# Performance work log

Measured on AMD Instinct MI355X. Metric: run time of the kernel, lower is better.

Reference implementation:

```python
import jax, jax.numpy as jnp
import numpy as np

HEADS = 8
DIM_HEAD = 64
SCALE = DIM_HEAD ** -0.5


def setup_inputs() -> dict:
    key = jax.random.key(0)
    k1, k2, k3 = jax.random.split(key, 3)
    B, C, L = 4, 512, 2048
    h_dim = HEADS * DIM_HEAD  # 512
    x = jax.random.normal(k1, (B, C, L), dtype=jnp.float32)
    w_qkv = jax.random.normal(k2, (C, 3 * h_dim), dtype=jnp.float32) * (C ** -0.5)
    w_out = jax.random.normal(k3, (h_dim, C), dtype=jnp.float32) * (h_dim ** -0.5)
    b_out = jnp.zeros((C,), dtype=jnp.float32)
    return {"x": x, "w_qkv": w_qkv, "w_out": w_out, "b_out": b_out}


def reference(x, w_qkv, w_out, b_out):
    B, C, L = x.shape
    # pointwise conv (kernel size 1, no bias): [B,C,L] x [C,3hd] -> [B,3hd,L]
    qkv = jnp.einsum('bcl,cf->bfl', x, w_qkv)
    q, k, v = jnp.split(qkv, 3, axis=1)  # each [B, h*d, L]
    def to_heads(t):
        return t.reshape(B, HEADS, DIM_HEAD, L)  # b h d l
    q, k, v = to_heads(q), to_heads(k), to_heads(v)
    q = q * SCALE
    sim = jnp.einsum('bhdi,bhdj->bhij', q, k)  # [B,H,L,L]
    attn = jax.nn.softmax(sim, axis=-1)  # stable (max-subtract) softmax
    out = jnp.einsum('bhij,bhdj->bhid', attn, v)  # [B,H,L,D]
    # rearrange 'b h l c -> b (h c) l'
    out = out.transpose(0, 1, 3, 2).reshape(B, HEADS * DIM_HEAD, L)
    # to_out pointwise conv with bias: [B,hd,L] -> [B,C,L]
    return jnp.einsum('bcl,cf->bfl', out, w_out) + b_out[None, :, None]
```

## Files before the change

kernel.cpp:

```cpp
#include <hip/hip_runtime.h>


#define LDIM 2048
#define CDIM 512
#define BATCH 4

typedef __attribute__((ext_vector_type(8))) short s16x8;
typedef __attribute__((ext_vector_type(4))) float f32x4;
typedef __attribute__((ext_vector_type(4))) unsigned short u16x4;
typedef unsigned int u32;
typedef unsigned short u16;

__device__ __forceinline__ u16 f2b(float f) {
    unsigned u = __float_as_uint(f);
    u += 0x7fffu + ((u >> 16) & 1u);
    return (u16)(u >> 16);
}
__device__ __forceinline__ u32 pk2(float a, float b) {
    u32 ua = __float_as_uint(a) + 0x8000u;
    u32 ub = __float_as_uint(b) + 0x8000u;
    return __builtin_amdgcn_perm(ub, ua, 0x07060302u);
}

__global__ __launch_bounds__(256)
void transpA_k(const float* __restrict__ x, const float* __restrict__ wq,
               const float* __restrict__ wo, u16* __restrict__ XP,
               u16* __restrict__ WP, u16* __restrict__ WOP)
{
    const int r0 = blockIdx.x * 64;
    const int y  = blockIdx.y;
    const float* in; u16* out; int inLD, c0;
    if (y < 128) {
        const int b = y >> 5, ct = y & 31;
        in = x + (size_t)b * CDIM * LDIM; inLD = LDIM; c0 = ct * 64;
        out = XP + (size_t)b * LDIM * CDIM;
    } else if (y < 152) {
        in = wq; inLD = 1536; c0 = (y - 128) * 64; out = WP;
    } else {
        in = wo; inLD = 512;  c0 = (y - 152) * 64; out = WOP;
    }

    __shared__ __align__(16) u16 t[64][80];
    const int tt = threadIdx.x;
    const int lr = tt >> 4, lc = (tt & 15) * 4;
    #pragma unroll
    for (int i = 0; i < 4; ++i) {
        f32x4 v = *(const f32x4*)(in + (size_t)(r0 + lr + i * 16) * inLD + c0 + lc);
        #pragma unroll
        for (int j = 0; j < 4; ++j) t[lc + j][lr + i * 16] = f2b(v[j]);
    }
    __syncthreads();
    const int orow = tt >> 2, ocg = (tt & 3) * 16;
    s16x8 v0 = *(const s16x8*)&t[orow][ocg];
    s16x8 v1 = *(const s16x8*)&t[orow][ocg + 8];
    const int row   = c0 + orow;
    const int rtile = row >> 4, rr = row & 15;
    const int cstep = (r0 + ocg) >> 5;
    const int qb    = (ocg >> 3) & 3;
    u16* dst = out + ((size_t)(rtile * 16 + cstep) * 64 + qb * 16 + rr) * 8;
    *(s16x8*)dst = v0;
    *(s16x8*)(dst + 128) = v1;
}

__global__ __launch_bounds__(256)
void qkvgemm_bf16(const u16* __restrict__ XP, const u16* __restrict__ WP,
                  u16* __restrict__ QF, u16* __restrict__ KF, u16* __restrict__ VF)
{
    const int f0 = blockIdx.x * 64;
    const int l0 = blockIdx.y * 128;
    const int b  = blockIdx.z;
    const u16* xTb = XP + (size_t)b * LDIM * CDIM;
    const int t = threadIdx.x, w = t >> 6, lane = t & 63;
    const int mn = lane & 15, q = lane >> 4;
    const bool vpart = (f0 >= 1024);

    const u16 *Abase, *Bbase;
    int mbase, nbase;
    if (!vpart) {
        mbase = f0 + (w >> 1) * 32; nbase = l0 + (w & 1) * 64;
        Abase = WP + (size_t)mbase * CDIM; Bbase = xTb + (size_t)nbase * CDIM;
    } else {
        mbase = l0 + w * 32; nbase = f0;
        Abase = xTb + (size_t)mbase * CDIM; Bbase = WP + (size_t)nbase * CDIM;
    }

    f32x4 acc[2][4] = {};
    #pragma unroll 2
    for (int c0 = 0; c0 < CDIM; c0 += 32) {
        s16x8 a[2], bf[4];
        #pragma unroll
        for (int mi = 0; mi < 2; ++mi)
            a[mi] = *(const s16x8*)(Abase + mi * 16 * CDIM + c0 * 16 + lane * 8);
        #pragma unroll
        for (int ni = 0; ni < 4; ++ni)
            bf[ni] = *(const s16x8*)(Bbase + ni * 16 * CDIM + c0 * 16 + lane * 8);
        #pragma unroll
        for (int mi = 0; mi < 2; ++mi)
            #pragma unroll
            for (int ni = 0; ni < 4; ++ni)
                acc[mi][ni] = __builtin_amdgcn_mfma_f32_16x16x32_bf16(a[mi], bf[ni], acc[mi][ni], 0, 0, 0);
    }

    if (!vpart) {
        const int part = f0 >> 9;
        const float sc2 = (part == 0) ? 0.18033688f : 1.0f;
        u16* Tout = (part == 0) ? QF : KF;
        #pragma unroll
        for (int mi = 0; mi < 2; ++mi) {
            const int fg0 = mbase + mi * 16;
            const int h = (fg0 >> 6) & 7;
            const int d0 = (fg0 & 63) + q * 4;
            const int kd = d0 >> 5, qq = (d0 >> 3) & 3, e0 = d0 & 7;
            u16* T = Tout + (size_t)(b * 8 + h) * LDIM * 64;
            #pragma unroll
            for (int ni = 0; ni < 4; ++ni) {
                const int lg = nbase + ni * 16 + mn;
                size_t addr;
                if (part == 0) {
                    const int t16 = lg >> 4, mnq = lg & 15;
                    addr = (size_t)((t16 * 2 + kd) * 512 + (qq * 16 + mnq) * 8 + e0);
                } else {
                    const int j64 = lg >> 6, r6 = lg & 63;
                    const int jt  = ((r6 >> 2) & 1) * 2 + (r6 >> 5);
                    const int mnk = ((r6 >> 3) & 3) * 4 + (r6 & 3);
                    addr = (size_t)(((j64 * 4 + jt) * 2 + kd) * 512 + (qq * 16 + mnk) * 8 + e0);
                }
                u16x4 pk;
                #pragma unroll
                for (int r = 0; r < 4; ++r) pk[r] = f2b(acc[mi][ni][r] * sc2);
                *(u16x4*)(T + addr) = pk;
            }
        }
    } else {
        #pragma unroll
        for (int ni = 0; ni < 4; ++ni) {
            const int fg = nbase + ni * 16 + mn;
            const int h = (fg >> 6) & 7;
            const int d = fg & 63;
            const int dt = d >> 4, mnv = d & 15;
            u16* Vb = VF + (size_t)(b * 8 + h) * LDIM * 64;
            #pragma unroll
            for (int mi = 0; mi < 2; ++mi) {
                const int lg0 = mbase + mi * 16 + q * 4;
                const int j64 = lg0 >> 6, j6 = lg0 & 63;
                const int kj = j6 >> 5, qq = (j6 >> 3) & 3, e0 = j6 & 7;
                const size_t addr = (size_t)(((j64 * 2 + kj) * 4 + dt) * 512 + (qq * 16 + mnv) * 8 + e0);
                u16x4 pk;
                #pragma unroll
                for (int r = 0; r < 4; ++r) pk[r] = f2b(acc[mi][ni][r]);
                *(u16x4*)(Vb + addr) = pk;
            }
        }
    }
}

__global__ __launch_bounds__(256)
void attn_k(const u16* __restrict__ QF, const u16* __restrict__ KF,
            const u16* __restrict__ VF, u16* __restrict__ aoP)
{
    const int bh = blockIdx.x;
    const int b = bh >> 3, h = bh & 7;
    const u16* Qh = QF + (size_t)bh * LDIM * 64;
    const u16* Kh = KF + (size_t)bh * LDIM * 64;
    const u16* Vh = VF + (size_t)bh * LDIM * 64;

    __shared__ __align__(16) float o_sh[3][64][68];
    __shared__ float lp_sh[3][64];

    const int tid = threadIdx.x;
    const int wv = tid >> 6;
    const int lane = tid & 63;
    const int mn = lane & 15, q = lane >> 4;
    const int ib64 = blockIdx.y;
    const int TH = 8;
    const int tbase = wv * TH;

    s16x8 aq[4][2];
    #pragma unroll
    for (int ibt = 0; ibt < 4; ++ibt) {
        const int t16 = ib64 * 4 + ibt;
        #pragma unroll
        for (int kd = 0; kd < 2; ++kd)
            aq[ibt][kd] = *(const s16x8*)(Qh + (size_t)((t16 * 2 + kd) * 512) + lane * 8);
    }

    f32x4 o_acc[4][4] = {};
    float lp[4] = {0.f, 0.f, 0.f, 0.f};

    s16x8 kc[2][4];
    {
        const u16* Kt = Kh + (size_t)tbase * 4096;
        #pragma unroll
        for (int kd = 0; kd < 2; ++kd)
            #pragma unroll
            for (int jt = 0; jt < 4; ++jt)
                kc[kd][jt] = *(const s16x8*)(Kt + ((jt * 2 + kd) << 9) + (lane << 3));
    }

    #pragma unroll 2
    for (int jj = 0; jj < TH; ++jj) {
        const int tn = tbase + ((jj + 1) & (TH - 1));
        const u16* Kt = Kh + (size_t)tn * 4096;
        const u16* Vt = Vh + (size_t)(tbase + jj) * 4096;

        s16x8 kn[2][4];
        #pragma unroll
        for (int kd = 0; kd < 2; ++kd)
            #pragma unroll
            for (int jt = 0; jt < 4; ++jt)
                kn[kd][jt] = *(const s16x8*)(Kt + ((jt * 2 + kd) << 9) + (lane << 3));

        f32x4 s[4][4] = {};
        #pragma unroll
        for (int kd = 0; kd < 2; ++kd)
            #pragma unroll
            for (int jt = 0; jt < 4; ++jt)
                #pragma unroll
                for (int ibt = 0; ibt < 4; ++ibt)
                    s[ibt][jt] = __builtin_amdgcn_mfma_f32_16x16x32_bf16(kc[kd][jt], aq[ibt][kd], s[ibt][jt], 0, 0, 0);

        s16x8 vc[2][4];
        #pragma unroll
        for (int kj = 0; kj < 2; ++kj)
            #pragma unroll
            for (int dt = 0; dt < 4; ++dt)
                vc[kj][dt] = *(const s16x8*)(Vt + ((kj * 4 + dt) << 9) + (lane << 3));

        #pragma unroll
        for (int kj = 0; kj < 2; ++kj) {
            s16x8 ap[4];
            #pragma unroll
            for (int ibt = 0; ibt < 4; ++ibt) {
                float pa0 = __builtin_amdgcn_exp2f(s[ibt][kj][0]);
                float pa1 = __builtin_amdgcn_exp2f(s[ibt][kj][1]);
                float pa2 = __builtin_amdgcn_exp2f(s[ibt][kj][2]);
                float pa3 = __builtin_amdgcn_exp2f(s[ibt][kj][3]);
                float pb0 = __builtin_amdgcn_exp2f(s[ibt][kj + 2][0]);
                float pb1 = __builtin_amdgcn_exp2f(s[ibt][kj + 2][1]);
                float pb2 = __builtin_amdgcn_exp2f(s[ibt][kj + 2][2]);
                float pb3 = __builtin_amdgcn_exp2f(s[ibt][kj + 2][3]);
                lp[ibt] += ((pa0 + pa1) + (pa2 + pa3)) + ((pb0 + pb1) + (pb2 + pb3));
                union { s16x8 v; u32 w[4]; } u;
                u.w[0] = pk2(pa0, pa1);
                u.w[1] = pk2(pa2, pa3);
                u.w[2] = pk2(pb0, pb1);
                u.w[3] = pk2(pb2, pb3);
                ap[ibt] = u.v;
            }
            #pragma unroll
            for (int dt = 0; dt < 4; ++dt)
                #pragma unroll
                for (int ibt = 0; ibt < 4; ++ibt)
                    o_acc[ibt][dt] = __builtin_amdgcn_mfma_f32_16x16x32_bf16(vc[kj][dt], ap[ibt], o_acc[ibt][dt], 0, 0, 0);
        }

        #pragma unroll
        for (int kd = 0; kd < 2; ++kd)
            #pragma unroll
            for (int jt = 0; jt < 4; ++jt)
                kc[kd][jt] = kn[kd][jt];
    }

    #pragma unroll
    for (int ibt = 0; ibt < 4; ++ibt) {
        lp[ibt] += __shfl_xor(lp[ibt], 16);
        lp[ibt] += __shfl_xor(lp[ibt], 32);
    }

    if (wv != 0) {
        #pragma unroll
        for (int ibt = 0; ibt < 4; ++ibt) {
            #pragma unroll
            for (int dt = 0; dt < 4; ++dt)
                *(f32x4*)&o_sh[wv - 1][ibt * 16 + mn][dt * 16 + q * 4] = o_acc[ibt][dt];
            if (q == 0) lp_sh[wv - 1][ibt * 16 + mn] = lp[ibt];
        }
    }
    __syncthreads();
    if (wv == 0) {
        u16* Ab = aoP + (size_t)b * LDIM * 512;
        #pragma unroll
        for (int ibt = 0; ibt < 4; ++ibt) {
            const int row = ibt * 16 + mn;
            const float lptot = lp[ibt] + lp_sh[0][row] + lp_sh[1][row] + lp_sh[2][row];
            const float rinv = 1.0f / lptot;
            const int ltile = ib64 * 4 + ibt;
            #pragma unroll
            for (int dt = 0; dt < 4; ++dt) {
                f32x4 o0 = *(const f32x4*)&o_sh[0][row][dt * 16 + q * 4];
                f32x4 o1 = *(const f32x4*)&o_sh[1][row][dt * 16 + q * 4];
                f32x4 o2 = *(const f32x4*)&o_sh[2][row][dt * 16 + q * 4];
                u16x4 pk;
                #pragma unroll
                for (int r = 0; r < 4; ++r)
                    pk[r] = f2b((o_acc[ibt][dt][r] + o0[r] + o1[r] + o2[r]) * rinv);
                const int cstep = h * 2 + (dt >> 1);
                const int lanep = ((dt & 1) * 2 + (q >> 1)) * 16 + mn;
                u16* dst = Ab + ((size_t)(ltile * 16 + cstep) * 64 + lanep) * 8 + (q & 1) * 4;
                *(u16x4*)dst = pk;
            }
        }
    }
}

__global__ __launch_bounds__(256)
void outgemm_d(const u16* __restrict__ aoP, const u16* __restrict__ WOP,
               const float* __restrict__ bias, float* __restrict__ Y)
{
    const int f0 = blockIdx.x * 64;
    const int l0 = blockIdx.y * 128;
    const int b  = blockIdx.z;
    const int t = threadIdx.x, w = t >> 6, lane = t & 63;
    const int mn = lane & 15, q = lane >> 4;
    const int mbase = f0 + (w >> 1) * 32;
    const int nbase = l0 + (w & 1) * 64;
    const u16* Abase = WOP + (size_t)mbase * CDIM;
    const u16* Bbase = aoP + ((size_t)b * LDIM + nbase) * CDIM;
    float* Yb = Y + (size_t)b * CDIM * LDIM;

    f32x4 acc[2][4] = {};
    #pragma unroll 2
    for (int c0 = 0; c0 < CDIM; c0 += 32) {
        s16x8 a[2], bf[4];
        #pragma unroll
        for (int mi = 0; mi < 2; ++mi)
            a[mi] = *(const s16x8*)(Abase + mi * 16 * CDIM + c0 * 16 + lane * 8);
        #pragma unroll
        for (int ni = 0; ni < 4; ++ni)
            bf[ni] = *(const s16x8*)(Bbase + ni * 16 * CDIM + c0 * 16 + lane * 8);
        #pragma unroll
        for (int mi = 0; mi < 2; ++mi)
            #pragma unroll
            for (int ni = 0; ni < 4; ++ni)
                acc[mi][ni] = __builtin_amdgcn_mfma_f32_16x16x32_bf16(a[mi], bf[ni], acc[mi][ni], 0, 0, 0);
    }
    #pragma unroll
    for (int mi = 0; mi < 2; ++mi)
        #pragma unroll
        for (int r = 0; r < 4; ++r) {
            const int f = mbase + mi * 16 + q * 4 + r;
            const float bs = bias[f];
            #pragma unroll
            for (int ni = 0; ni < 4; ++ni)
                Yb[(size_t)f * LDIM + nbase + ni * 16 + mn] = acc[mi][ni][r] + bs;
        }
}

extern "C" void kernel_launch(void* const* d_in, const int* in_sizes, int n_in,
                              void* d_out, int out_size, void* d_ws, size_t ws_size,
                              hipStream_t stream) {
    const float *x = nullptr, *w_qkv = nullptr, *w_out = nullptr, *b_out = nullptr;
    for (int i = 0; i < n_in; ++i) {
        switch (in_sizes[i]) {
            case 4 * 512 * 2048: x     = (const float*)d_in[i]; break;
            case 512 * 1536:     w_qkv = (const float*)d_in[i]; break;
            case 512 * 512:      w_out = (const float*)d_in[i]; break;
            case 512:            b_out = (const float*)d_in[i]; break;
        }
    }
    float* out = (float*)d_out;

    const size_t SLAB = (size_t)BATCH * LDIM * 512;
    u16* WOP = (u16*)d_ws;
    u16* XP  = WOP + (size_t)512 * 512;
    u16* WP  = XP + SLAB;
    u16* QF  = WP + (size_t)1536 * 512;
    u16* KF  = QF + SLAB;
    u16* VF  = KF + SLAB;
    u16* aoP = VF + SLAB;

    transpA_k<<<dim3(8, 160), 256, 0, stream>>>(x, w_qkv, w_out, XP, WP, WOP);
    qkvgemm_bf16<<<dim3(24, 16, BATCH), 256, 0, stream>>>(XP, WP, QF, KF, VF);
    attn_k<<<dim3(32, 32), 256, 0, stream>>>(QF, KF, VF, aoP);
    outgemm_d<<<dim3(8, 16, BATCH), 256, 0, stream>>>(aoP, WOP, b_out, out);
}
```

Measured before the change: 178.9 us.

## Software-pipeline attention loop so PV MFMAs overlap next tile's exp

Restructures the inner attention loop into a prologue, a steady state and an epilogue. The QK^T product and exp of tile j+1 are now interleaved with the PV MFMAs of tile j, and the K and V loads are issued one stage ahead. The aim is to hide exp/pack VALU latency and global-load latency behind matrix-core work. The cost is more live registers (ap, apn, vc, kc), which risks lower occupancy or spills. The loop is also no longer unrolled by 2.

```diff
diff --git a/kernel.cpp b/kernel.cpp
--- a/kernel.cpp
+++ b/kernel.cpp
@@ -187,7 +187,8 @@
     f32x4 o_acc[4][4] = {};
     float lp[4] = {0.f, 0.f, 0.f, 0.f};
 
-    s16x8 kc[2][4];
+    s16x8 kc[2][4], vc[2][4], ap[2][4];
+
     {
         const u16* Kt = Kh + (size_t)tbase * 4096;
         #pragma unroll
@@ -195,20 +196,6 @@
             #pragma unroll
             for (int jt = 0; jt < 4; ++jt)
                 kc[kd][jt] = *(const s16x8*)(Kt + ((jt * 2 + kd) << 9) + (lane << 3));
-    }
-
-    #pragma unroll 2
-    for (int jj = 0; jj < TH; ++jj) {
-        const int tn = tbase + ((jj + 1) & (TH - 1));
-        const u16* Kt = Kh + (size_t)tn * 4096;
-        const u16* Vt = Vh + (size_t)(tbase + jj) * 4096;
-
-        s16x8 kn[2][4];
-        #pragma unroll
-        for (int kd = 0; kd < 2; ++kd)
-            #pragma unroll
-            for (int jt = 0; jt < 4; ++jt)
-                kn[kd][jt] = *(const s16x8*)(Kt + ((jt * 2 + kd) << 9) + (lane << 3));
 
         f32x4 s[4][4] = {};
         #pragma unroll
@@ -219,7 +206,13 @@
                 for (int ibt = 0; ibt < 4; ++ibt)
                     s[ibt][jt] = __builtin_amdgcn_mfma_f32_16x16x32_bf16(kc[kd][jt], aq[ibt][kd], s[ibt][jt], 0, 0, 0);
 
-        s16x8 vc[2][4];
+        const u16* Ktn = Kh + (size_t)(tbase + 1) * 4096;
+        #pragma unroll
+        for (int kd = 0; kd < 2; ++kd)
+            #pragma unroll
+            for (int jt = 0; jt < 4; ++jt)
+                kc[kd][jt] = *(const s16x8*)(Ktn + ((jt * 2 + kd) << 9) + (lane << 3));
+        const u16* Vt = Vh + (size_t)tbase * 4096;
         #pragma unroll
         for (int kj = 0; kj < 2; ++kj)
             #pragma unroll
@@ -227,8 +220,7 @@
                 vc[kj][dt] = *(const s16x8*)(Vt + ((kj * 4 + dt) << 9) + (lane << 3));
 
         #pragma unroll
-        for (int kj = 0; kj < 2; ++kj) {
-            s16x8 ap[4];
+        for (int kj = 0; kj < 2; ++kj)
             #pragma unroll
             for (int ibt = 0; ibt < 4; ++ibt) {
                 float pa0 = __builtin_amdgcn_exp2f(s[ibt][kj][0]);
@@ -245,21 +237,77 @@
                 u.w[1] = pk2(pa2, pa3);
                 u.w[2] = pk2(pb0, pb1);
                 u.w[3] = pk2(pb2, pb3);
-                ap[ibt] = u.v;
+                ap[kj][ibt] = u.v;
             }
+    }
+
+    for (int jj = 0; jj < TH - 1; ++jj) {
+        f32x4 s[4][4] = {};
+        #pragma unroll
+        for (int kd = 0; kd < 2; ++kd)
+            #pragma unroll
+            for (int jt = 0; jt < 4; ++jt)
+                #pragma unroll
+                for (int ibt = 0; ibt < 4; ++ibt)
+                    s[ibt][jt] = __builtin_amdgcn_mfma_f32_16x16x32_bf16(kc[kd][jt], aq[ibt][kd], s[ibt][jt], 0, 0, 0);
+
+        {
+            const u16* Ktn = Kh + (size_t)(tbase + ((jj + 2) & (TH - 1))) * 4096;
+            #pragma unroll
+            for (int kd = 0; kd < 2; ++kd)
+                #pragma unroll
+                for (int jt = 0; jt < 4; ++jt)
+                    kc[kd][jt] = *(const s16x8*)(Ktn + ((jt * 2 + kd) << 9) + (lane << 3));
+        }
+
+        s16x8 apn[2][4];
+        #pragma unroll
+        for (int kj = 0; kj < 2; ++kj)
+            #pragma unroll
+            for (int ibt = 0; ibt < 4; ++ibt) {
+                float pa0 = __builtin_amdgcn_exp2f(s[ibt][kj][0]);
+                float pa1 = __builtin_amdgcn_exp2f(s[ibt][kj][1]);
+                float pa2 = __builtin_amdgcn_exp2f(s[ibt][kj][2]);
+                float pa3 = __builtin_amdgcn_exp2f(s[ibt][kj][3]);
+                float pb0 = __builtin_amdgcn_exp2f(s[ibt][kj + 2][0]);
+                float pb1 = __builtin_amdgcn_exp2f(s[ibt][kj + 2][1]);
+                float pb2 = __builtin_amdgcn_exp2f(s[ibt][kj + 2][2]);
+                float pb3 = __builtin_amdgcn_exp2f(s[ibt][kj + 2][3]);
+                lp[ibt] += ((pa0 + pa1) + (pa2 + pa3)) + ((pb0 + pb1) + (pb2 + pb3));
+                union { s16x8 v; u32 w[4]; } u;
+                u.w[0] = pk2(pa0, pa1);
+                u.w[1] = pk2(pa2, pa3);
+                u.w[2] = pk2(pb0, pb1);
+                u.w[3] = pk2(pb2, pb3);
+                apn[kj][ibt] = u.v;
+                #pragma unroll
+                for (int dt = 0; dt < 4; ++dt)
+                    o_acc[ibt][dt] = __builtin_amdgcn_mfma_f32_16x16x32_bf16(vc[kj][dt], ap[kj][ibt], o_acc[ibt][dt], 0, 0, 0);
+            }
+
+        {
+            const u16* Vtn = Vh + (size_t)(tbase + jj + 1) * 4096;
+            #pragma unroll
+            for (int kj = 0; kj < 2; ++kj)
+                #pragma unroll
+                for (int dt = 0; dt < 4; ++dt)
+                    vc[kj][dt] = *(const s16x8*)(Vtn + ((kj * 4 + dt) << 9) + (lane << 3));
+        }
+
+        #pragma unroll
+        for (int kj = 0; kj < 2; ++kj)
+            #pragma unroll
+            for (int ibt = 0; ibt < 4; ++ibt)
+                ap[kj][ibt] = apn[kj][ibt];
+    }
+
+    #pragma unroll
+    for (int kj = 0; kj < 2; ++kj)
+        #pragma unroll
+        for (int ibt = 0; ibt < 4; ++ibt)
             #pragma unroll
             for (int dt = 0; dt < 4; ++dt)
-                #pragma unroll
-                for (int ibt = 0; ibt < 4; ++ibt)
-                    o_acc[ibt][dt] = __builtin_amdgcn_mfma_f32_16x16x32_bf16(vc[kj][dt], ap[ibt], o_acc[ibt][dt], 0, 0, 0);
-        }
-
-        #pragma unroll
-        for (int kd = 0; kd < 2; ++kd)
-            #pragma unroll
-            for (int jt = 0; jt < 4; ++jt)
-                kc[kd][jt] = kn[kd][jt];
-    }
+                o_acc[ibt][dt] = __builtin_amdgcn_mfma_f32_16x16x32_bf16(vc[kj][dt], ap[kj][ibt], o_acc[ibt][dt], 0, 0, 0);
 
     #pragma unroll
     for (int ibt = 0; ibt < 4; ++ibt) {
```

Result: no change. 175.9 us (-1.7%).
